# Kernel tuning notes

Hardware: AMD Instinct MI355X
Metric: run time of the kernel (lower is better)

The kernel has to match this reference:

```python
import jax, jax.numpy as jnp
import numpy as np

B, L, D = 2, 1024, 768
NL = 8            # n_layers
DI = 2 * D        # d_inner (expand=2)
NS = 16           # d_state
DR = D // 16      # dt_rank = 48
KC = 4            # d_conv
EPS = 1e-5


def setup_inputs() -> dict:
    key = jax.random.key(0)
    ks = jax.random.split(key, 12)
    s = 0.02
    inp = {
        "x":        jax.random.normal(ks[0], (B, L, D), jnp.float32),
        "ln_w":     jnp.ones((NL, D), jnp.float32),
        "ln_b":     jnp.zeros((NL, D), jnp.float32),
        "in_proj":  jax.random.normal(ks[1], (NL, 2 * DI, D), jnp.float32) * s,
        "conv_w":   jax.random.normal(ks[2], (NL, DI, KC), jnp.float32) * 0.1,
        "conv_b":   jnp.zeros((NL, DI), jnp.float32),
        "x_proj":   jax.random.normal(ks[3], (NL, DR + 2 * NS, DI), jnp.float32) * s,
        "dt_w":     jax.random.normal(ks[4], (NL, DI, DR), jnp.float32) * s,
        "dt_b":     jax.random.normal(ks[5], (NL, DI), jnp.float32) * 0.5,
        "A_log":    jnp.broadcast_to(jnp.log(jnp.arange(1, NS + 1, dtype=jnp.float32)), (NL, DI, NS)).copy(),
        "D_skip":   jnp.ones((NL, DI), jnp.float32),
        "out_proj": jax.random.normal(ks[6], (NL, D, DI), jnp.float32) * s,
        "fn_w":     jnp.ones((D,), jnp.float32),
        "fn_b":     jnp.zeros((D,), jnp.float32),
    }
    return inp


def _layernorm(x, w, b):
    mu = x.mean(-1, keepdims=True)
    var = ((x - mu) ** 2).mean(-1, keepdims=True)
    return (x - mu) * jax.lax.rsqrt(var + EPS) * w + b


def _silu(x):
    return x * jax.nn.sigmoid(x)


def _mamba(xn, Wi, cw, cb, Wx, Wdt, bdt, A_log, Dp, Wo):
    # xn: (B, L, D)
    xz = jnp.einsum('bld,ed->ble', xn, Wi)          # (B, L, 2*DI)
    xi, z = jnp.split(xz, 2, axis=-1)               # each (B, L, DI)
    # causal depthwise conv along L
    xc = jax.lax.conv_general_dilated(
        xi.transpose(0, 2, 1), cw[:, None, :], (1,), [(KC - 1, 0)],
        feature_group_count=DI, dimension_numbers=('NCH', 'OIH', 'NCH'))
    xc = _silu(xc.transpose(0, 2, 1) + cb)          # (B, L, DI)
    dbc = jnp.einsum('ble,re->blr', xc, Wx)         # (B, L, DR+2*NS)
    dt = jax.nn.softplus(jnp.einsum('blr,dr->bld', dbc[..., :DR], Wdt) + bdt)  # (B,L,DI)
    Bm = dbc[..., DR:DR + NS]                        # (B, L, NS)
    Cm = dbc[..., DR + NS:]                          # (B, L, NS)
    A = -jnp.exp(A_log)                              # (DI, NS)

    def step(h, inp):
        dt_t, B_t, C_t, x_t = inp                    # (B,DI),(B,NS),(B,NS),(B,DI)
        dA = jnp.exp(dt_t[..., None] * A)            # (B, DI, NS)
        h = dA * h + (dt_t * x_t)[..., None] * B_t[:, None, :]
        y = jnp.einsum('bdn,bn->bd', h, C_t)
        return h, y

    xs = (dt.transpose(1, 0, 2), Bm.transpose(1, 0, 2),
          Cm.transpose(1, 0, 2), xc.transpose(1, 0, 2))
    h0 = jnp.zeros((xn.shape[0], DI, NS), xn.dtype)
    _, ys = jax.lax.scan(step, h0, xs)               # ys: (L, B, DI)
    y = ys.transpose(1, 0, 2) + xc * Dp
    y = y * _silu(z)
    return jnp.einsum('ble,de->bld', y, Wo)          # (B, L, D)


def reference(x, ln_w, ln_b, in_proj, conv_w, conv_b, x_proj, dt_w, dt_b,
              A_log, D_skip, out_proj, fn_w, fn_b):
    params = (ln_w, ln_b, in_proj, conv_w, conv_b, x_proj, dt_w, dt_b,
              A_log, D_skip, out_proj)

    def block(carry, p):
        xcur, res = carry
        lw, lb, Wi, cw, cb, Wx, Wdt, bdt, Al, Dp, Wo = p
        res = xcur + res                 # residual = x + residual
        xn = _layernorm(xcur, lw, lb)    # norm(x) -- note: norms block input, per source
        h = _mamba(xn, Wi, cw, cb, Wx, Wdt, bdt, Al, Dp, Wo)
        return (h, res), None

    res0 = jnp.zeros_like(x)             # residual=None handled as zeros
    (xf, resf), _ = jax.lax.scan(block, (x, res0), params)
    out = _layernorm(xf + resf, fn_w, fn_b)
    return out
```

## Files before the change

### kernel.cpp

```cpp
#include <hip/hip_runtime.h>
#include <math.h>

#define B_ 2
#define L_ 1024
#define D_ 768
#define NL_ 8
#define DI_ 1536
#define NS_ 16
#define DR_ 48
#define KC_ 4
#define EPS_ 1e-5f
#define M_ (B_*L_)
#define NC_ 32
#define T_ 32
#define KS_ 16
#define KCH_ (DI_/KS_)
#define KDT_ 64

typedef short bf16x8 __attribute__((ext_vector_type(8)));
typedef float f32x4  __attribute__((ext_vector_type(4)));

__device__ __forceinline__ unsigned short f2bf(float f) {
    union { float f; unsigned int u; } v; v.f = f;
    unsigned int u = v.u;
    u += 0x7fffu + ((u >> 16) & 1u);
    return (unsigned short)(u >> 16);
}

__device__ __forceinline__ unsigned int pk2(float a, float b) {
    union { float f; unsigned int u; } va, vb;
    va.f = a; vb.f = b;
    unsigned int ua = va.u + (0x7fffu + ((va.u >> 16) & 1u));
    unsigned int ub = vb.u + (0x7fffu + ((vb.u >> 16) & 1u));
    return (ua >> 16) | (ub & 0xffff0000u);
}

__device__ __forceinline__ void gload16(const void* g, void* l) {
    __builtin_amdgcn_global_load_lds(
        (const __attribute__((address_space(1))) void*)g,
        (__attribute__((address_space(3))) void*)l, 16, 0, 0);
}

__device__ __forceinline__ void cvt_blk(const float* __restrict__ s,
                                        unsigned short* __restrict__ d, int tid) {
    int o = tid * 4;
    float4 a0 = *(const float4*)&s[o];
    float4 a1 = *(const float4*)&s[o + 1024];
    float4 a2 = *(const float4*)&s[o + 2048];
    float4 a3 = *(const float4*)&s[o + 3072];
    *(uint2*)&d[o]        = (uint2){pk2(a0.x, a0.y), pk2(a0.z, a0.w)};
    *(uint2*)&d[o + 1024] = (uint2){pk2(a1.x, a1.y), pk2(a1.z, a1.w)};
    *(uint2*)&d[o + 2048] = (uint2){pk2(a2.x, a2.y), pk2(a2.z, a2.w)};
    *(uint2*)&d[o + 3072] = (uint2){pk2(a3.x, a3.y), pk2(a3.z, a3.w)};
}

__global__ __launch_bounds__(256) void prep_kernel(
    const float* __restrict__ wi, unsigned short* __restrict__ wi_bf,
    const float* __restrict__ wo, unsigned short* __restrict__ wo_bf,
    const float* __restrict__ wx, unsigned short* __restrict__ wx_bf,
    const float* __restrict__ wdt, unsigned short* __restrict__ wdt_bf,
    const float* __restrict__ A_log, float* __restrict__ negA,
    const float* __restrict__ x, float* __restrict__ xcur,
    float* __restrict__ res,
    unsigned short* __restrict__ dbc_bf) {
    const int E0 = NL_ * 2 * DI_ * D_;
    const int E1 = NL_ * D_ * DI_;
    const int E2 = NL_ * 80 * DI_;
    const int E3 = NL_ * DI_ * KDT_;
    const int E4 = NL_ * DI_ * NS_;
    const int E5 = M_ * D_;
    int tid = threadIdx.x;
    int base = blockIdx.x * 4096;
    if (base < E0) { cvt_blk(wi + base, wi_bf + base, tid); return; }
    base -= E0;
    if (base < E1) { cvt_blk(wo + base, wo_bf + base, tid); return; }
    base -= E1;
    if (base < E2) { cvt_blk(wx + base, wx_bf + base, tid); return; }
    base -= E2;
    if (base < E3) {
        int off0 = base + tid * 4;
        int col = off0 & (KDT_ - 1);
        if (col < DR_) {
            float4 a0 = *(const float4*)&wdt[(size_t)((off0) >> 6) * DR_ + col];
            float4 a1 = *(const float4*)&wdt[(size_t)((off0 + 1024) >> 6) * DR_ + col];
            float4 a2 = *(const float4*)&wdt[(size_t)((off0 + 2048) >> 6) * DR_ + col];
            float4 a3 = *(const float4*)&wdt[(size_t)((off0 + 3072) >> 6) * DR_ + col];
            *(uint2*)&wdt_bf[off0]        = (uint2){pk2(a0.x, a0.y), pk2(a0.z, a0.w)};
            *(uint2*)&wdt_bf[off0 + 1024] = (uint2){pk2(a1.x, a1.y), pk2(a1.z, a1.w)};
            *(uint2*)&wdt_bf[off0 + 2048] = (uint2){pk2(a2.x, a2.y), pk2(a2.z, a2.w)};
            *(uint2*)&wdt_bf[off0 + 3072] = (uint2){pk2(a3.x, a3.y), pk2(a3.z, a3.w)};
        } else {
            uint2 z = {0u, 0u};
            *(uint2*)&wdt_bf[off0] = z;
            *(uint2*)&wdt_bf[off0 + 1024] = z;
            *(uint2*)&wdt_bf[off0 + 2048] = z;
            *(uint2*)&wdt_bf[off0 + 3072] = z;
        }
        return;
    }
    base -= E3;
    if (base < E4) {
        int off0 = base + tid * 4;
        float4 a0 = *(const float4*)&A_log[off0];
        float4 a1 = *(const float4*)&A_log[off0 + 1024];
        float4 a2 = *(const float4*)&A_log[off0 + 2048];
        float4 a3 = *(const float4*)&A_log[off0 + 3072];
        *(float4*)&negA[off0] = make_float4(-__expf(a0.x), -__expf(a0.y), -__expf(a0.z), -__expf(a0.w));
        *(float4*)&negA[off0 + 1024] = make_float4(-__expf(a1.x), -__expf(a1.y), -__expf(a1.z), -__expf(a1.w));
        *(float4*)&negA[off0 + 2048] = make_float4(-__expf(a2.x), -__expf(a2.y), -__expf(a2.z), -__expf(a2.w));
        *(float4*)&negA[off0 + 3072] = make_float4(-__expf(a3.x), -__expf(a3.y), -__expf(a3.z), -__expf(a3.w));
        return;
    }
    base -= E4;
    if (base < E5) {
        int off0 = base + tid * 4;
        float4 a0 = *(const float4*)&x[off0];
        float4 a1 = *(const float4*)&x[off0 + 1024];
        float4 a2 = *(const float4*)&x[off0 + 2048];
        float4 a3 = *(const float4*)&x[off0 + 3072];
        float4 z = make_float4(0.f, 0.f, 0.f, 0.f);
        *(float4*)&xcur[off0] = a0;        *(float4*)&res[off0] = z;
        *(float4*)&xcur[off0 + 1024] = a1; *(float4*)&res[off0 + 1024] = z;
        *(float4*)&xcur[off0 + 2048] = a2; *(float4*)&res[off0 + 2048] = z;
        *(float4*)&xcur[off0 + 3072] = a3; *(float4*)&res[off0 + 3072] = z;
        return;
    }
    base -= E5;
    {
        int off0 = base + tid * 4;
        uint2 z = {0u, 0u};
        *(uint2*)&dbc_bf[off0] = z;
        *(uint2*)&dbc_bf[off0 + 1024] = z;
        *(uint2*)&dbc_bf[off0 + 2048] = z;
        *(uint2*)&dbc_bf[off0 + 3072] = z;
    }
}

__device__ __forceinline__ float wave_sum(float v) {
    #pragma unroll
    for (int o = 32; o > 0; o >>= 1) v += __shfl_down(v, o);
    return __shfl(v, 0);
}

__global__ __launch_bounds__(256) void ln_res_kernel(
    const float* __restrict__ xcur, float* __restrict__ res,
    const float* __restrict__ w, const float* __restrict__ b,
    unsigned short* __restrict__ xn) {
    int wave = threadIdx.x >> 6, lane = threadIdx.x & 63;
    int row = blockIdx.x * 4 + wave;
    size_t base = (size_t)row * D_;
    int off = lane * 4;
    float4 v0 = *(const float4*)&xcur[base + off];
    float4 v1 = *(const float4*)&xcur[base + off + 256];
    float4 v2 = *(const float4*)&xcur[base + off + 512];
    float4 r0 = *(const float4*)&res[base + off];
    float4 r1 = *(const float4*)&res[base + off + 256];
    float4 r2 = *(const float4*)&res[base + off + 512];
    r0.x += v0.x; r0.y += v0.y; r0.z += v0.z; r0.w += v0.w;
    r1.x += v1.x; r1.y += v1.y; r1.z += v1.z; r1.w += v1.w;
    r2.x += v2.x; r2.y += v2.y; r2.z += v2.z; r2.w += v2.w;
    *(float4*)&res[base + off]       = r0;
    *(float4*)&res[base + off + 256] = r1;
    *(float4*)&res[base + off + 512] = r2;
    float s = (v0.x + v0.y + v0.z + v0.w) + (v1.x + v1.y + v1.z + v1.w)
            + (v2.x + v2.y + v2.z + v2.w);
    float mu = wave_sum(s) * (1.0f / D_);
    float4 d0 = make_float4(v0.x - mu, v0.y - mu, v0.z - mu, v0.w - mu);
    float4 d1 = make_float4(v1.x - mu, v1.y - mu, v1.z - mu, v1.w - mu);
    float4 d2 = make_float4(v2.x - mu, v2.y - mu, v2.z - mu, v2.w - mu);
    float sv = d0.x * d0.x + d0.y * d0.y + d0.z * d0.z + d0.w * d0.w
             + d1.x * d1.x + d1.y * d1.y + d1.z * d1.z + d1.w * d1.w
             + d2.x * d2.x + d2.y * d2.y + d2.z * d2.z + d2.w * d2.w;
    float var = wave_sum(sv) * (1.0f / D_);
    float rs = rsqrtf(var + EPS_);
    float4 w0 = *(const float4*)&w[off];
    float4 w1 = *(const float4*)&w[off + 256];
    float4 w2 = *(const float4*)&w[off + 512];
    float4 b0 = *(const float4*)&b[off];
    float4 b1 = *(const float4*)&b[off + 256];
    float4 b2 = *(const float4*)&b[off + 512];
    *(uint2*)&xn[base + off] = (uint2){
        pk2(d0.x * rs * w0.x + b0.x, d0.y * rs * w0.y + b0.y),
        pk2(d0.z * rs * w0.z + b0.z, d0.w * rs * w0.w + b0.w)};
    *(uint2*)&xn[base + off + 256] = (uint2){
        pk2(d1.x * rs * w1.x + b1.x, d1.y * rs * w1.y + b1.y),
        pk2(d1.z * rs * w1.z + b1.z, d1.w * rs * w1.w + b1.w)};
    *(uint2*)&xn[base + off + 512] = (uint2){
        pk2(d2.x * rs * w2.x + b2.x, d2.y * rs * w2.y + b2.y),
        pk2(d2.z * rs * w2.z + b2.z, d2.w * rs * w2.w + b2.w)};
}

__global__ __launch_bounds__(256) void final_ln_kernel(
    const float* __restrict__ xcur, const float* __restrict__ res,
    const float* __restrict__ w, const float* __restrict__ b,
    float* __restrict__ out) {
    int wave = threadIdx.x >> 6, lane = threadIdx.x & 63;
    int row = blockIdx.x * 4 + wave;
    size_t base = (size_t)row * D_;
    int off = lane * 4;
    float4 v0 = *(const float4*)&xcur[base + off];
    float4 v1 = *(const float4*)&xcur[base + off + 256];
    float4 v2 = *(const float4*)&xcur[base + off + 512];
    float4 r0 = *(const float4*)&res[base + off];
    float4 r1 = *(const float4*)&res[base + off + 256];
    float4 r2 = *(const float4*)&res[base + off + 512];
    v0.x += r0.x; v0.y += r0.y; v0.z += r0.z; v0.w += r0.w;
    v1.x += r1.x; v1.y += r1.y; v1.z += r1.z; v1.w += r1.w;
    v2.x += r2.x; v2.y += r2.y; v2.z += r2.z; v2.w += r2.w;
    float s = (v0.x + v0.y + v0.z + v0.w) + (v1.x + v1.y + v1.z + v1.w)
            + (v2.x + v2.y + v2.z + v2.w);
    float mu = wave_sum(s) * (1.0f / D_);
    float4 d0 = make_float4(v0.x - mu, v0.y - mu, v0.z - mu, v0.w - mu);
    float4 d1 = make_float4(v1.x - mu, v1.y - mu, v1.z - mu, v1.w - mu);
    float4 d2 = make_float4(v2.x - mu, v2.y - mu, v2.z - mu, v2.w - mu);
    float sv = d0.x * d0.x + d0.y * d0.y + d0.z * d0.z + d0.w * d0.w
             + d1.x * d1.x + d1.y * d1.y + d1.z * d1.z + d1.w * d1.w
             + d2.x * d2.x + d2.y * d2.y + d2.z * d2.z + d2.w * d2.w;
    float var = wave_sum(sv) * (1.0f / D_);
    float rs = rsqrtf(var + EPS_);
    float4 w0 = *(const float4*)&w[off];
    float4 w1 = *(const float4*)&w[off + 256];
    float4 w2 = *(const float4*)&w[off + 512];
    float4 b0 = *(const float4*)&b[off];
    float4 b1 = *(const float4*)&b[off + 256];
    float4 b2 = *(const float4*)&b[off + 512];
    *(float4*)&out[base + off] = make_float4(
        d0.x * rs * w0.x + b0.x, d0.y * rs * w0.y + b0.y,
        d0.z * rs * w0.z + b0.z, d0.w * rs * w0.w + b0.w);
    *(float4*)&out[base + off + 256] = make_float4(
        d1.x * rs * w1.x + b1.x, d1.y * rs * w1.y + b1.y,
        d1.z * rs * w1.z + b1.z, d1.w * rs * w1.w + b1.w);
    *(float4*)&out[base + off + 512] = make_float4(
        d2.x * rs * w2.x + b2.x, d2.y * rs * w2.y + b2.y,
        d2.z * rs * w2.z + b2.z, d2.w * rs * w2.w + b2.w);
}

template <int BM, int BN>
__global__ __launch_bounds__(256) void gemm_bf16_t(
    const unsigned short* __restrict__ A,
    const unsigned short* __restrict__ W,
    float* __restrict__ C, int M, int N, int K) {
    constexpr int FM = BM / 32;
    constexpr int FN = BN / 32;
    constexpr int NLD = (BM + BN) / 64;
    __shared__ unsigned short sA[BM * 32];
    __shared__ unsigned short sW[BN * 32];
    int bm = blockIdx.y * BM, bn = blockIdx.x * BN;
    int tid = threadIdx.x;
    int wave = tid >> 6, lane = tid & 63;
    int wrow = (wave & 1) * (BM / 2), wcol = (wave >> 1) * (BN / 2);
    int quad = lane >> 4, r16 = lane & 15;
    f32x4 acc[FM][FN];
    #pragma unroll
    for (int i = 0; i < FM; i++)
        #pragma unroll
        for (int j = 0; j < FN; j++)
            acc[i][j] = (f32x4){0.f, 0.f, 0.f, 0.f};

    for (int k0 = 0; k0 < K; k0 += 32) {
        #pragma unroll
        for (int r = 0; r < NLD; r++) {
            if (r < BM / 64) {
                int j = r * 256 + tid;
                gload16(&A[(size_t)(bm + (j >> 2)) * K + k0 + (j & 3) * 8],
                        &sA[(r * 256 + wave * 64) * 8]);
            } else {
                int j = (r - BM / 64) * 256 + tid;
                gload16(&W[(size_t)(bn + (j >> 2)) * K + k0 + (j & 3) * 8],
                        &sW[((r - BM / 64) * 256 + wave * 64) * 8]);
            }
        }
        __syncthreads();
        bf16x8 af[FM], wf[FN];
        #pragma unroll
        for (int i = 0; i < FM; i++)
            af[i] = *(const bf16x8*)&sA[(wrow + i * 16 + r16) * 32 + quad * 8];
        #pragma unroll
        for (int j = 0; j < FN; j++)
            wf[j] = *(const bf16x8*)&sW[(wcol + j * 16 + r16) * 32 + quad * 8];
        #pragma unroll
        for (int i = 0; i < FM; i++)
            #pragma unroll
            for (int j = 0; j < FN; j++)
                acc[i][j] = __builtin_amdgcn_mfma_f32_16x16x32_bf16(
                    af[i], wf[j], acc[i][j], 0, 0, 0);
        __syncthreads();
    }
    #pragma unroll
    for (int i = 0; i < FM; i++) {
        #pragma unroll
        for (int j = 0; j < FN; j++) {
            int col = bn + wcol + j * 16 + r16;
            #pragma unroll
            for (int reg = 0; reg < 4; reg++) {
                int row = bm + wrow + i * 16 + quad * 4 + reg;
                C[(size_t)row * N + col] = acc[i][j][reg];
            }
        }
    }
}

__global__ __launch_bounds__(256) void dt_gemm_bf16(
    const unsigned short* __restrict__ A,
    const unsigned short* __restrict__ W,
    const float* __restrict__ bias,
    float* __restrict__ dtb) {
    __shared__ unsigned short sA[128 * 32];
    __shared__ unsigned short sW[128 * 32];
    int bm = blockIdx.y * 128, bn = blockIdx.x * 128;
    int tid = threadIdx.x;
    int wave = tid >> 6, lane = tid & 63;
    int wrow = (wave & 1) * 64, wcol = (wave >> 1) * 64;
    int quad = lane >> 4, r16 = lane & 15;
    f32x4 acc[4][4];
    #pragma unroll
    for (int i = 0; i < 4; i++)
        #pragma unroll
        for (int j = 0; j < 4; j++)
            acc[i][j] = (f32x4){0.f, 0.f, 0.f, 0.f};

    #pragma unroll
    for (int k0 = 0; k0 < KDT_; k0 += 32) {
        #pragma unroll
        for (int r = 0; r < 4; r++) {
            if (r < 2) {
                int j = r * 256 + tid;
                gload16(&A[(size_t)(bm + (j >> 2)) * KDT_ + k0 + (j & 3) * 8],
                        &sA[(r * 256 + wave * 64) * 8]);
            } else {
                int j = (r - 2) * 256 + tid;
                gload16(&W[(size_t)(bn + (j >> 2)) * KDT_ + k0 + (j & 3) * 8],
                        &sW[((r - 2) * 256 + wave * 64) * 8]);
            }
        }
        __syncthreads();
        bf16x8 af[4], wf[4];
        #pragma unroll
        for (int i = 0; i < 4; i++)
            af[i] = *(const bf16x8*)&sA[(wrow + i * 16 + r16) * 32 + quad * 8];
        #pragma unroll
        for (int j = 0; j < 4; j++)
            wf[j] = *(const bf16x8*)&sW[(wcol + j * 16 + r16) * 32 + quad * 8];
        #pragma unroll
        for (int i = 0; i < 4; i++)
            #pragma unroll
            for (int j = 0; j < 4; j++)
                acc[i][j] = __builtin_amdgcn_mfma_f32_16x16x32_bf16(
                    af[i], wf[j], acc[i][j], 0, 0, 0);
        __syncthreads();
    }
    #pragma unroll
    for (int i = 0; i < 4; i++) {
        #pragma unroll
        for (int j = 0; j < 4; j++) {
            int col = bn + wcol + j * 16 + r16;
            float bv = bias[col];
            #pragma unroll
            for (int reg = 0; reg < 4; reg++) {
                int row = bm + wrow + i * 16 + quad * 4 + reg;
                float v = acc[i][j][reg] + bv;
                v = (v > 20.f) ? v : log1pf(__expf(v));
                dtb[(size_t)row * DI_ + col] = v;
            }
        }
    }
}

__global__ __launch_bounds__(256) void conv_xproj_kernel(
    const float* __restrict__ xz,
    const float* __restrict__ cw,
    const float* __restrict__ cb,
    const unsigned short* __restrict__ W,
    float* __restrict__ xcf,
    float* __restrict__ Pb) {
    __shared__ float sxz[67 * 96];
    __shared__ unsigned short sxcb[64 * 104];
    __shared__ float scw[96 * 4];
    __shared__ float scb[96];
    unsigned short* sW = (unsigned short*)sxz;

    int ks = blockIdx.x;
    int bm = blockIdx.y * 64;
    int tid = threadIdx.x;
    int b = bm >> 10, t0 = bm & (L_ - 1);
    int dbase = ks * KCH_;

    if (tid < 96) {
        int d = dbase + tid;
        *(float4*)&scw[tid * 4] = *(const float4*)&cw[d * 4];
        scb[tid] = cb[d];
    }
    for (int j = tid; j < 67 * 24; j += 256) {
        int r = j / 24, c4 = (j % 24) * 4;
        int tt = t0 + r - 3;
        float4 v = make_float4(0.f, 0.f, 0.f, 0.f);
        if (tt >= 0)
            v = *(const float4*)&xz[((size_t)(b * L_ + tt)) * (2 * DI_) + dbase + c4];
        *(float4*)&sxz[r * 96 + c4] = v;
    }
    __syncthreads();
    for (int j = tid; j < 64 * 96; j += 256) {
        int r = j / 96, c = j % 96;
        float acc = scb[c];
        #pragma unroll
        for (int k = 0; k < KC_; k++)
            acc = fmaf(scw[c * 4 + k], sxz[(r + k) * 96 + c], acc);
        float v = acc / (1.0f + __expf(-acc));
        xcf[(size_t)(bm + r) * DI_ + dbase + c] = v;
        sxcb[r * 104 + c] = f2bf(v);
    }
    __syncthreads();
    for (int j = tid; j < 80 * 12; j += 256) {
        int row = j / 12, c16 = (j % 12) * 8;
        *(uint4*)&sW[row * 104 + c16] =
            *(const uint4*)&W[(size_t)row * DI_ + dbase + c16];
    }
    __syncthreads();
    int wave = tid >> 6, lane = tid & 63;
    int quad = lane >> 4, r16 = lane & 15;
    f32x4 acc[5];
    #pragma unroll
    for (int j = 0; j < 5; j++) acc[j] = (f32x4){0.f, 0.f, 0.f, 0.f};
    #pragma unroll
    for (int kk = 0; kk < 3; kk++) {
        bf16x8 af = *(const bf16x8*)&sxcb[(wave * 16 + r16) * 104 + kk * 32 + quad * 8];
        #pragma unroll
        for (int j = 0; j < 5; j++) {
            bf16x8 wf = *(const bf16x8*)&sW[(j * 16 + r16) * 104 + kk * 32 + quad * 8];
            acc[j] = __builtin_amdgcn_mfma_f32_16x16x32_bf16(af, wf, acc[j], 0, 0, 0);
        }
    }
    #pragma unroll
    for (int j = 0; j < 5; j++) {
        int col = j * 16 + r16;
        #pragma unroll
        for (int reg = 0; reg < 4; reg++) {
            int row = bm + wave * 16 + quad * 4 + reg;
            Pb[((size_t)ks * M_ + row) * 80 + col] = acc[j][reg];
        }
    }
}

__global__ void xproj_reduce_kernel(const float* __restrict__ Pb,
                                    unsigned short* __restrict__ dbc_bf,
                                    float* __restrict__ bcp) {
    int i = blockIdx.x * 256 + threadIdx.x;
    float s = 0.f;
    #pragma unroll
    for (int ks = 0; ks < KS_; ks++) s += Pb[(size_t)ks * (M_ * 80) + i];
    int m = i / 80, col = i % 80;
    if (col < DR_) {
        dbc_bf[m * KDT_ + col] = f2bf(s);
    } else if (col < DR_ + NS_) {
        bcp[m * 32 + 2 * (col - DR_)] = s;
    } else {
        bcp[m * 32 + 2 * (col - DR_ - NS_) + 1] = s;
    }
}

__global__ __launch_bounds__(128) void scan_ps_kernel(
    const float* __restrict__ dtb,
    const float* __restrict__ xcf,
    const float4* __restrict__ bcp4,
    const float* __restrict__ negA,
    float* __restrict__ Sb,
    float* __restrict__ sdb) {
    const int NDB = DI_ / 128;
    int bx = blockIdx.x;
    int dblk = bx % NDB;
    int c = (bx / NDB) % NC_;
    int b = bx / (NDB * NC_);
    int d = dblk * 128 + threadIdx.x;

    float A[NS_];
    #pragma unroll
    for (int n = 0; n < NS_; n++) A[n] = negA[(size_t)d * NS_ + n];
    float h[NS_];
    #pragma unroll
    for (int n = 0; n < NS_; n++) h[n] = 0.f;
    float sd = 0.f;

    size_t btbase = (size_t)(b * L_ + c * T_);
    const float* pdt = dtb + btbase * DI_ + d;
    const float* pxc = xcf + btbase * DI_ + d;
    const float4* pbc = bcp4 + btbase * 8;

    #pragma unroll 4
    for (int t = 0; t < T_; t++) {
        float dt = pdt[(size_t)t * DI_];
        float u  = dt * pxc[(size_t)t * DI_];
        sd += dt;
        #pragma unroll
        for (int q = 0; q < 8; q++) {
            float4 v = pbc[t * 8 + q];
            float e0 = __expf(dt * A[2 * q]);
            h[2 * q] = fmaf(e0, h[2 * q], u * v.x);
            float e1 = __expf(dt * A[2 * q + 1]);
            h[2 * q + 1] = fmaf(e1, h[2 * q + 1], u * v.z);
        }
    }

    size_t o = (((size_t)b * NC_ + c) * DI_ + d) * NS_;
    #pragma unroll
    for (int n = 0; n < NS_; n++) Sb[o + n] = h[n];
    sdb[((size_t)b * NC_ + c) * DI_ + d] = sd;
}

__global__ __launch_bounds__(64) void scan_combine_kernel(
    const float* __restrict__ Sb, const float* __restrict__ sdb,
    const float* __restrict__ negA, float* __restrict__ hin) {
    int i = blockIdx.x * 64 + threadIdx.x;
    int b = i / (DI_ * NS_);
    int rem = i % (DI_ * NS_);
    int d = rem >> 4;
    float Aa = negA[rem];
    const size_t str = (size_t)DI_ * NS_;
    size_t o = (size_t)b * NC_ * str + rem;
    size_t osd = (size_t)b * NC_ * DI_ + d;
    float h = 0.f;
    float s0 = Sb[o],           sd0 = sdb[osd];
    float s1 = Sb[o + str],     sd1 = sdb[osd + DI_];
    float s2 = Sb[o + 2 * str], sd2 = sdb[osd + 2 * DI_];
    float s3 = Sb[o + 3 * str], sd3 = sdb[osd + 3 * DI_];
    for (int c = 0; c < NC_ - 4; c += 4) {
        float n0 = Sb[o + 4 * str], nd0 = sdb[osd + 4 * DI_];
        float n1 = Sb[o + 5 * str], nd1 = sdb[osd + 5 * DI_];
        float n2 = Sb[o + 6 * str], nd2 = sdb[osd + 6 * DI_];
        float n3 = Sb[o + 7 * str], nd3 = sdb[osd + 7 * DI_];
        hin[o] = h;           h = fmaf(__expf(Aa * sd0), h, s0);
        hin[o + str] = h;     h = fmaf(__expf(Aa * sd1), h, s1);
        hin[o + 2 * str] = h; h = fmaf(__expf(Aa * sd2), h, s2);
        hin[o + 3 * str] = h; h = fmaf(__expf(Aa * sd3), h, s3);
        s0 = n0; sd0 = nd0; s1 = n1; sd1 = nd1;
        s2 = n2; sd2 = nd2; s3 = n3; sd3 = nd3;
        o += 4 * str; osd += 4 * DI_;
    }
    hin[o] = h;           h = fmaf(__expf(Aa * sd0), h, s0);
    hin[o + str] = h;     h = fmaf(__expf(Aa * sd1), h, s1);
    hin[o + 2 * str] = h; h = fmaf(__expf(Aa * sd2), h, s2);
    hin[o + 3 * str] = h;
}

__global__ __launch_bounds__(128) void scan_out_kernel(
    const float* __restrict__ dtb, const float* __restrict__ xcf,
    const float4* __restrict__ bcp4, const float* __restrict__ negA,
    const float* __restrict__ hin, const float* __restrict__ xz,
    const float* __restrict__ Dp, unsigned short* __restrict__ yg) {
    const int NDB = DI_ / 128;
    int bx = blockIdx.x;
    int dblk = bx % NDB;
    int c = (bx / NDB) % NC_;
    int b = bx / (NDB * NC_);
    int d = dblk * 128 + threadIdx.x;

    float A[NS_];
    #pragma unroll
    for (int n = 0; n < NS_; n++) A[n] = negA[(size_t)d * NS_ + n];
    size_t o = (((size_t)b * NC_ + c) * DI_ + d) * NS_;
    float h[NS_];
    #pragma unroll
    for (int n = 0; n < NS_; n++) h[n] = hin[o + n];
    float dpv = Dp[d];

    size_t btbase = (size_t)(b * L_ + c * T_);
    const float* pdt = dtb + btbase * DI_ + d;
    const float* pxc = xcf + btbase * DI_ + d;
    const float4* pbc = bcp4 + btbase * 8;

    #pragma unroll 4
    for (int t = 0; t < T_; t++) {
        float dt = pdt[(size_t)t * DI_];
        float xc = pxc[(size_t)t * DI_];
        float u = dt * xc;
        float y = 0.f;
        #pragma unroll
        for (int q = 0; q < 8; q++) {
            float4 v = pbc[t * 8 + q];
            float e0 = __expf(dt * A[2 * q]);
            h[2 * q] = fmaf(e0, h[2 * q], u * v.x);
            y = fmaf(v.y, h[2 * q], y);
            float e1 = __expf(dt * A[2 * q + 1]);
            h[2 * q + 1] = fmaf(e1, h[2 * q + 1], u * v.z);
            y = fmaf(v.w, h[2 * q + 1], y);
        }
        size_t row = btbase + t;
        float zv = xz[row * (2 * DI_) + DI_ + d];
        float yy = y + xc * dpv;
        yy *= zv / (1.0f + __expf(-zv));
        yg[row * DI_ + d] = f2bf(yy);
    }
}

extern "C" void kernel_launch(void* const* d_in, const int* in_sizes, int n_in,
                              void* d_out, int out_size, void* d_ws, size_t ws_size,
                              hipStream_t stream) {
    const float* x        = (const float*)d_in[0];
    const float* ln_w     = (const float*)d_in[1];
    const float* ln_b     = (const float*)d_in[2];
    const float* in_proj  = (const float*)d_in[3];
    const float* conv_w   = (const float*)d_in[4];
    const float* conv_b   = (const float*)d_in[5];
    const float* x_proj   = (const float*)d_in[6];
    const float* dt_w     = (const float*)d_in[7];
    const float* dt_b     = (const float*)d_in[8];
    const float* A_log    = (const float*)d_in[9];
    const float* D_skip   = (const float*)d_in[10];
    const float* out_proj = (const float*)d_in[11];
    const float* fn_w     = (const float*)d_in[12];
    const float* fn_b     = (const float*)d_in[13];
    float* out = (float*)d_out;

    char* p = (char*)d_ws;
    auto alloc = [&](size_t bytes) {
        char* r = p;
        p += (bytes + 255) & ~(size_t)255;
        return (void*)r;
    };
    float* xcur = (float*)alloc((size_t)M_ * D_ * 4);
    float* res  = (float*)alloc((size_t)M_ * D_ * 4);
    unsigned short* xn = (unsigned short*)alloc((size_t)M_ * D_ * 2);
    float* xz   = (float*)alloc((size_t)M_ * 2 * DI_ * 4);
    float* dtb  = (float*)alloc((size_t)M_ * DI_ * 4);
    float* xcf  = (float*)alloc((size_t)M_ * DI_ * 4);
    unsigned short* dbc_bf = (unsigned short*)alloc((size_t)M_ * KDT_ * 2);
    float* bcp  = (float*)alloc((size_t)M_ * 32 * 4);
    unsigned short* yg = (unsigned short*)alloc((size_t)M_ * DI_ * 2);
    float* Sb   = (float*)alloc((size_t)B_ * NC_ * DI_ * NS_ * 4);
    float* sdb  = (float*)alloc((size_t)B_ * NC_ * DI_ * 4);
    float* hin  = (float*)alloc((size_t)B_ * NC_ * DI_ * NS_ * 4);
    float* Pb   = (float*)alloc((size_t)KS_ * M_ * 80 * 4);
    float* negA = (float*)alloc((size_t)NL_ * DI_ * NS_ * 4);
    const size_t n_wi = (size_t)NL_ * 2 * DI_ * D_;
    const size_t n_wo = (size_t)NL_ * D_ * DI_;
    const size_t n_wx = (size_t)NL_ * 80 * DI_;
    const size_t n_wdt = (size_t)NL_ * DI_ * KDT_;
    unsigned short* wi_bf = (unsigned short*)alloc(n_wi * 2);
    unsigned short* wo_bf = (unsigned short*)alloc(n_wo * 2);
    unsigned short* wx_bf = (unsigned short*)alloc(n_wx * 2);
    unsigned short* wdt_bf = (unsigned short*)alloc(n_wdt * 2);

    prep_kernel<<<7808, 256, 0, stream>>>(
        in_proj, wi_bf, out_proj, wo_bf, x_proj, wx_bf,
        dt_w, wdt_bf, A_log, negA, x, xcur, res, dbc_bf);

    for (int l = 0; l < NL_; l++) {
        const float* negA_l = negA + (size_t)l * DI_ * NS_;

        ln_res_kernel<<<M_ / 4, 256, 0, stream>>>(
            xcur, res, ln_w + l * D_, ln_b + l * D_, xn);

        gemm_bf16_t<128, 64><<<dim3((2 * DI_) / 64, M_ / 128), 256, 0, stream>>>(
            xn, wi_bf + (size_t)l * 2 * DI_ * D_, xz, M_, 2 * DI_, D_);

        conv_xproj_kernel<<<dim3(KS_, M_ / 64), 256, 0, stream>>>(
            xz, conv_w + l * DI_ * KC_, conv_b + l * DI_,
            wx_bf + (size_t)l * 80 * DI_, xcf, Pb);
        xproj_reduce_kernel<<<(M_ * 80) / 256, 256, 0, stream>>>(Pb, dbc_bf, bcp);

        dt_gemm_bf16<<<dim3(DI_ / 128, M_ / 128), 256, 0, stream>>>(
            dbc_bf, wdt_bf + (size_t)l * DI_ * KDT_, dt_b + l * DI_, dtb);

        scan_ps_kernel<<<B_ * NC_ * (DI_ / 128), 128, 0, stream>>>(
            dtb, xcf, (const float4*)bcp, negA_l, Sb, sdb);
        scan_combine_kernel<<<(B_ * DI_ * NS_) / 64, 64, 0, stream>>>(
            Sb, sdb, negA_l, hin);
        scan_out_kernel<<<B_ * NC_ * (DI_ / 128), 128, 0, stream>>>(
            dtb, xcf, (const float4*)bcp, negA_l, hin, xz,
            D_skip + (size_t)l * DI_, yg);

        gemm_bf16_t<64, 64><<<dim3(D_ / 64, M_ / 64), 256, 0, stream>>>(
            yg, wo_bf + (size_t)l * D_ * DI_, xcur, M_, D_, DI_);
    }

    final_ln_kernel<<<M_ / 4, 256, 0, stream>>>(xcur, res, fn_w, fn_b, out);
}
```

Baseline: 1.281 ms.

## Fuse three scan phases into one cooperative kernel with grid syncs

Merges the chunk-local scan, the cross-chunk combine and the output scan into a single cooperative launch. Grid-wide barriers replace the two kernel boundaries that separated the phases. The grid is 768 blocks of 128 threads, which must all be co-resident for the cooperative launch. The combine phase now runs with 128 threads per block over the same 768 blocks, which covers all 49152 state elements. This saves two launches per layer, at the cost of grid-sync overhead and possible launch failure or lower occupancy if residency limits are exceeded.

```diff
diff --git a/kernel.cpp b/kernel.cpp
--- a/kernel.cpp
+++ b/kernel.cpp
@@ -1,5 +1,8 @@
 #include <hip/hip_runtime.h>
+#include <hip/hip_cooperative_groups.h>
 #include <math.h>
+
+namespace cg = cooperative_groups;
 
 #define B_ 2
 #define L_ 1024
@@ -458,13 +461,13 @@
     }
 }
 
-__global__ __launch_bounds__(128) void scan_ps_kernel(
-    const float* __restrict__ dtb,
-    const float* __restrict__ xcf,
-    const float4* __restrict__ bcp4,
-    const float* __restrict__ negA,
-    float* __restrict__ Sb,
-    float* __restrict__ sdb) {
+__global__ __launch_bounds__(128) void scan_fused_kernel(
+    const float* __restrict__ dtb, const float* __restrict__ xcf,
+    const float4* __restrict__ bcp4, const float* __restrict__ negA,
+    float* __restrict__ Sb, float* __restrict__ sdb,
+    float* __restrict__ hin, const float* __restrict__ xz,
+    const float* __restrict__ Dp, unsigned short* __restrict__ yg) {
+    cg::grid_group grid = cg::this_grid();
     const int NDB = DI_ / 128;
     int bx = blockIdx.x;
     int dblk = bx % NDB;
@@ -475,119 +478,104 @@
     float A[NS_];
     #pragma unroll
     for (int n = 0; n < NS_; n++) A[n] = negA[(size_t)d * NS_ + n];
-    float h[NS_];
-    #pragma unroll
-    for (int n = 0; n < NS_; n++) h[n] = 0.f;
-    float sd = 0.f;
 
     size_t btbase = (size_t)(b * L_ + c * T_);
     const float* pdt = dtb + btbase * DI_ + d;
     const float* pxc = xcf + btbase * DI_ + d;
     const float4* pbc = bcp4 + btbase * 8;
 
-    #pragma unroll 4
-    for (int t = 0; t < T_; t++) {
-        float dt = pdt[(size_t)t * DI_];
-        float u  = dt * pxc[(size_t)t * DI_];
-        sd += dt;
-        #pragma unroll
-        for (int q = 0; q < 8; q++) {
-            float4 v = pbc[t * 8 + q];
-            float e0 = __expf(dt * A[2 * q]);
-            h[2 * q] = fmaf(e0, h[2 * q], u * v.x);
-            float e1 = __expf(dt * A[2 * q + 1]);
-            h[2 * q + 1] = fmaf(e1, h[2 * q + 1], u * v.z);
-        }
-    }
-
-    size_t o = (((size_t)b * NC_ + c) * DI_ + d) * NS_;
-    #pragma unroll
-    for (int n = 0; n < NS_; n++) Sb[o + n] = h[n];
-    sdb[((size_t)b * NC_ + c) * DI_ + d] = sd;
-}
-
-__global__ __launch_bounds__(64) void scan_combine_kernel(
-    const float* __restrict__ Sb, const float* __restrict__ sdb,
-    const float* __restrict__ negA, float* __restrict__ hin) {
-    int i = blockIdx.x * 64 + threadIdx.x;
-    int b = i / (DI_ * NS_);
-    int rem = i % (DI_ * NS_);
-    int d = rem >> 4;
-    float Aa = negA[rem];
-    const size_t str = (size_t)DI_ * NS_;
-    size_t o = (size_t)b * NC_ * str + rem;
-    size_t osd = (size_t)b * NC_ * DI_ + d;
-    float h = 0.f;
-    float s0 = Sb[o],           sd0 = sdb[osd];
-    float s1 = Sb[o + str],     sd1 = sdb[osd + DI_];
-    float s2 = Sb[o + 2 * str], sd2 = sdb[osd + 2 * DI_];
-    float s3 = Sb[o + 3 * str], sd3 = sdb[osd + 3 * DI_];
-    for (int c = 0; c < NC_ - 4; c += 4) {
-        float n0 = Sb[o + 4 * str], nd0 = sdb[osd + 4 * DI_];
-        float n1 = Sb[o + 5 * str], nd1 = sdb[osd + 5 * DI_];
-        float n2 = Sb[o + 6 * str], nd2 = sdb[osd + 6 * DI_];
-        float n3 = Sb[o + 7 * str], nd3 = sdb[osd + 7 * DI_];
-        hin[o] = h;           h = fmaf(__expf(Aa * sd0), h, s0);
-        hin[o + str] = h;     h = fmaf(__expf(Aa * sd1), h, s1);
-        hin[o + 2 * str] = h; h = fmaf(__expf(Aa * sd2), h, s2);
-        hin[o + 3 * str] = h; h = fmaf(__expf(Aa * sd3), h, s3);
-        s0 = n0; sd0 = nd0; s1 = n1; sd1 = nd1;
-        s2 = n2; sd2 = nd2; s3 = n3; sd3 = nd3;
-        o += 4 * str; osd += 4 * DI_;
-    }
-    hin[o] = h;           h = fmaf(__expf(Aa * sd0), h, s0);
-    hin[o + str] = h;     h = fmaf(__expf(Aa * sd1), h, s1);
-    hin[o + 2 * str] = h; h = fmaf(__expf(Aa * sd2), h, s2);
-    hin[o + 3 * str] = h;
-}
-
-__global__ __launch_bounds__(128) void scan_out_kernel(
-    const float* __restrict__ dtb, const float* __restrict__ xcf,
-    const float4* __restrict__ bcp4, const float* __restrict__ negA,
-    const float* __restrict__ hin, const float* __restrict__ xz,
-    const float* __restrict__ Dp, unsigned short* __restrict__ yg) {
-    const int NDB = DI_ / 128;
-    int bx = blockIdx.x;
-    int dblk = bx % NDB;
-    int c = (bx / NDB) % NC_;
-    int b = bx / (NDB * NC_);
-    int d = dblk * 128 + threadIdx.x;
-
-    float A[NS_];
-    #pragma unroll
-    for (int n = 0; n < NS_; n++) A[n] = negA[(size_t)d * NS_ + n];
-    size_t o = (((size_t)b * NC_ + c) * DI_ + d) * NS_;
-    float h[NS_];
-    #pragma unroll
-    for (int n = 0; n < NS_; n++) h[n] = hin[o + n];
-    float dpv = Dp[d];
-
-    size_t btbase = (size_t)(b * L_ + c * T_);
-    const float* pdt = dtb + btbase * DI_ + d;
-    const float* pxc = xcf + btbase * DI_ + d;
-    const float4* pbc = bcp4 + btbase * 8;
-
-    #pragma unroll 4
-    for (int t = 0; t < T_; t++) {
-        float dt = pdt[(size_t)t * DI_];
-        float xc = pxc[(size_t)t * DI_];
-        float u = dt * xc;
-        float y = 0.f;
-        #pragma unroll
-        for (int q = 0; q < 8; q++) {
-            float4 v = pbc[t * 8 + q];
-            float e0 = __expf(dt * A[2 * q]);
-            h[2 * q] = fmaf(e0, h[2 * q], u * v.x);
-            y = fmaf(v.y, h[2 * q], y);
-            float e1 = __expf(dt * A[2 * q + 1]);
-            h[2 * q + 1] = fmaf(e1, h[2 * q + 1], u * v.z);
-            y = fmaf(v.w, h[2 * q + 1], y);
-        }
-        size_t row = btbase + t;
-        float zv = xz[row * (2 * DI_) + DI_ + d];
-        float yy = y + xc * dpv;
-        yy *= zv / (1.0f + __expf(-zv));
-        yg[row * DI_ + d] = f2bf(yy);
+    {
+        float h[NS_];
+        #pragma unroll
+        for (int n = 0; n < NS_; n++) h[n] = 0.f;
+        float sd = 0.f;
+        #pragma unroll 4
+        for (int t = 0; t < T_; t++) {
+            float dt = pdt[(size_t)t * DI_];
+            float u  = dt * pxc[(size_t)t * DI_];
+            sd += dt;
+            #pragma unroll
+            for (int q = 0; q < 8; q++) {
+                float4 v = pbc[t * 8 + q];
+                float e0 = __expf(dt * A[2 * q]);
+                h[2 * q] = fmaf(e0, h[2 * q], u * v.x);
+                float e1 = __expf(dt * A[2 * q + 1]);
+                h[2 * q + 1] = fmaf(e1, h[2 * q + 1], u * v.z);
+            }
+        }
+        size_t o = (((size_t)b * NC_ + c) * DI_ + d) * NS_;
+        #pragma unroll
+        for (int n = 0; n < NS_; n++) Sb[o + n] = h[n];
+        sdb[((size_t)b * NC_ + c) * DI_ + d] = sd;
+    }
+
+    grid.sync();
+
+    {
+        int i = blockIdx.x * 128 + threadIdx.x;
+        if (i < B_ * DI_ * NS_) {
+            int bb = i / (DI_ * NS_);
+            int rem = i % (DI_ * NS_);
+            int dd = rem >> 4;
+            float Aa = negA[rem];
+            const size_t str = (size_t)DI_ * NS_;
+            size_t o = (size_t)bb * NC_ * str + rem;
+            size_t osd = (size_t)bb * NC_ * DI_ + dd;
+            float h = 0.f;
+            float s0 = Sb[o],           sd0 = sdb[osd];
+            float s1 = Sb[o + str],     sd1 = sdb[osd + DI_];
+            float s2 = Sb[o + 2 * str], sd2 = sdb[osd + 2 * DI_];
+            float s3 = Sb[o + 3 * str], sd3 = sdb[osd + 3 * DI_];
+            for (int cc = 0; cc < NC_ - 4; cc += 4) {
+                float n0 = Sb[o + 4 * str], nd0 = sdb[osd + 4 * DI_];
+                float n1 = Sb[o + 5 * str], nd1 = sdb[osd + 5 * DI_];
+                float n2 = Sb[o + 6 * str], nd2 = sdb[osd + 6 * DI_];
+                float n3 = Sb[o + 7 * str], nd3 = sdb[osd + 7 * DI_];
+                hin[o] = h;           h = fmaf(__expf(Aa * sd0), h, s0);
+                hin[o + str] = h;     h = fmaf(__expf(Aa * sd1), h, s1);
+                hin[o + 2 * str] = h; h = fmaf(__expf(Aa * sd2), h, s2);
+                hin[o + 3 * str] = h; h = fmaf(__expf(Aa * sd3), h, s3);
+                s0 = n0; sd0 = nd0; s1 = n1; sd1 = nd1;
+                s2 = n2; sd2 = nd2; s3 = n3; sd3 = nd3;
+                o += 4 * str; osd += 4 * DI_;
+            }
+            hin[o] = h;           h = fmaf(__expf(Aa * sd0), h, s0);
+            hin[o + str] = h;     h = fmaf(__expf(Aa * sd1), h, s1);
+            hin[o + 2 * str] = h; h = fmaf(__expf(Aa * sd2), h, s2);
+            hin[o + 3 * str] = h;
+        }
+    }
+
+    grid.sync();
+
+    {
+        size_t o = (((size_t)b * NC_ + c) * DI_ + d) * NS_;
+        float h[NS_];
+        #pragma unroll
+        for (int n = 0; n < NS_; n++) h[n] = hin[o + n];
+        float dpv = Dp[d];
+        #pragma unroll 4
+        for (int t = 0; t < T_; t++) {
+            float dt = pdt[(size_t)t * DI_];
+            float xc = pxc[(size_t)t * DI_];
+            float u = dt * xc;
+            float y = 0.f;
+            #pragma unroll
+            for (int q = 0; q < 8; q++) {
+                float4 v = pbc[t * 8 + q];
+                float e0 = __expf(dt * A[2 * q]);
+                h[2 * q] = fmaf(e0, h[2 * q], u * v.x);
+                y = fmaf(v.y, h[2 * q], y);
+                float e1 = __expf(dt * A[2 * q + 1]);
+                h[2 * q + 1] = fmaf(e1, h[2 * q + 1], u * v.z);
+                y = fmaf(v.w, h[2 * q + 1], y);
+            }
+            size_t row = btbase + t;
+            float zv = xz[row * (2 * DI_) + DI_ + d];
+            float yy = y + xc * dpv;
+            yy *= zv / (1.0f + __expf(-zv));
+            yg[row * DI_ + d] = f2bf(yy);
+        }
     }
 }
 
@@ -645,6 +633,7 @@
 
     for (int l = 0; l < NL_; l++) {
         const float* negA_l = negA + (size_t)l * DI_ * NS_;
+        const float* Dp_l = D_skip + (size_t)l * DI_;
 
         ln_res_kernel<<<M_ / 4, 256, 0, stream>>>(
             xcur, res, ln_w + l * D_, ln_b + l * D_, xn);
@@ -660,13 +649,15 @@
         dt_gemm_bf16<<<dim3(DI_ / 128, M_ / 128), 256, 0, stream>>>(
             dbc_bf, wdt_bf + (size_t)l * DI_ * KDT_, dt_b + l * DI_, dtb);
 
-        scan_ps_kernel<<<B_ * NC_ * (DI_ / 128), 128, 0, stream>>>(
-            dtb, xcf, (const float4*)bcp, negA_l, Sb, sdb);
-        scan_combine_kernel<<<(B_ * DI_ * NS_) / 64, 64, 0, stream>>>(
-            Sb, sdb, negA_l, hin);
-        scan_out_kernel<<<B_ * NC_ * (DI_ / 128), 128, 0, stream>>>(
-            dtb, xcf, (const float4*)bcp, negA_l, hin, xz,
-            D_skip + (size_t)l * DI_, yg);
+        {
+            const float4* bcp4 = (const float4*)bcp;
+            void* args[] = {
+                (void*)&dtb, (void*)&xcf, (void*)&bcp4, (void*)&negA_l,
+                (void*)&Sb, (void*)&sdb, (void*)&hin, (void*)&xz,
+                (void*)&Dp_l, (void*)&yg };
+            hipLaunchCooperativeKernel((void*)scan_fused_kernel,
+                dim3(B_ * NC_ * (DI_ / 128)), dim3(128), args, 0, stream);
+        }
 
         gemm_bf16_t<64, 64><<<dim3(D_ / 64, M_ / 64), 256, 0, stream>>>(
             yg, wo_bf + (size_t)l * D_ * DI_, xcur, M_, D_, DI_);
```

New measurement: 2.709 ms. 112% more time.
